# Performance work log

Measured on AMD Instinct MI355X. Metric: run time of the kernel, lower is better.

Reference implementation:

```python
import jax, jax.numpy as jnp
import numpy as np

D = 128
N_DRUG = 200000
N_PROT = 100000
E = 800000


def setup_inputs() -> dict:
    key = jax.random.key(0)
    ks = iter(jax.random.split(key, 64))
    inp = {}
    # initial node embeddings (nn.Embedding init: normal std=0.01)
    inp["x_drug"] = jax.random.normal(next(ks), (N_DRUG, D), jnp.float32) * 0.01
    inp["x_prot"] = jax.random.normal(next(ks), (N_PROT, D), jnp.float32) * 0.01
    # SAGEConv params per (layer, relation): lin_l (weight+bias), lin_r (weight, no bias)
    scale = 1.0 / np.sqrt(D)
    for l in (0, 1):
        for r in ("dp", "pd", "dd"):
            inp[f"Wl_{l}_{r}"] = jax.random.normal(next(ks), (D, D), jnp.float32) * scale
            inp[f"b_{l}_{r}"] = jnp.zeros((D,), jnp.float32)
            inp[f"Wr_{l}_{r}"] = jax.random.normal(next(ks), (D, D), jnp.float32) * scale
    # edge lists: (drug->protein), (protein->drug), (drug->drug)
    inp["e_dp_src"] = jax.random.randint(next(ks), (E,), 0, N_DRUG, dtype=jnp.int32)
    inp["e_dp_dst"] = jax.random.randint(next(ks), (E,), 0, N_PROT, dtype=jnp.int32)
    inp["e_pd_src"] = jax.random.randint(next(ks), (E,), 0, N_PROT, dtype=jnp.int32)
    inp["e_pd_dst"] = jax.random.randint(next(ks), (E,), 0, N_DRUG, dtype=jnp.int32)
    inp["e_dd_src"] = jax.random.randint(next(ks), (E,), 0, N_DRUG, dtype=jnp.int32)
    inp["e_dd_dst"] = jax.random.randint(next(ks), (E,), 0, N_DRUG, dtype=jnp.int32)
    return inp


def _sage(x_src, x_dst, src, dst, Wl, b, Wr):
    """PyG SAGEConv(aggr='mean'): lin_l(mean_neighbors) + lin_r(x_dst)."""
    n_dst = x_dst.shape[0]
    agg = jax.ops.segment_sum(x_src[src], dst, num_segments=n_dst)          # [n_dst, D]
    cnt = jax.ops.segment_sum(jnp.ones(src.shape, x_src.dtype), dst, num_segments=n_dst)
    mean = agg / jnp.maximum(cnt, 1.0)[:, None]  # isolated nodes -> 0
    return mean @ Wl.T + b + x_dst @ Wr.T


def _forward(xd, xp, params, edges):
    e_dp_s, e_dp_d, e_pd_s, e_pd_d, e_dd_s, e_dd_d = edges
    for l in (0, 1):
        p = params[l]
        # HeteroConv(aggr='sum'): sum SAGEConv outputs per destination node type
        new_p = _sage(xd, xp, e_dp_s, e_dp_d, *p["dp"])
        new_d = _sage(xp, xd, e_pd_s, e_pd_d, *p["pd"]) + _sage(xd, xd, e_dd_s, e_dd_d, *p["dd"])
        xd, xp = new_d, new_p
        if l == 0:  # relu (+ dropout as identity in eval) between layers only
            xd, xp = jax.nn.relu(xd), jax.nn.relu(xp)
    return jnp.concatenate([xd, xp], axis=0)  # [N_DRUG + N_PROT, D]


def reference(x_drug, x_prot,
              Wl_0_dp, b_0_dp, Wr_0_dp, Wl_0_pd, b_0_pd, Wr_0_pd, Wl_0_dd, b_0_dd, Wr_0_dd,
              Wl_1_dp, b_1_dp, Wr_1_dp, Wl_1_pd, b_1_pd, Wr_1_pd, Wl_1_dd, b_1_dd, Wr_1_dd,
              e_dp_src, e_dp_dst, e_pd_src, e_pd_dst, e_dd_src, e_dd_dst):
    params = [
        {"dp": (Wl_0_dp, b_0_dp, Wr_0_dp), "pd": (Wl_0_pd, b_0_pd, Wr_0_pd), "dd": (Wl_0_dd, b_0_dd, Wr_0_dd)},
        {"dp": (Wl_1_dp, b_1_dp, Wr_1_dp), "pd": (Wl_1_pd, b_1_pd, Wr_1_pd), "dd": (Wl_1_dd, b_1_dd, Wr_1_dd)},
    ]
    edges = (e_dp_src, e_dp_dst, e_pd_src, e_pd_dst, e_dd_src, e_dd_dst)
    return _forward(x_drug, x_prot, params, edges)
```

## Files before the change

kernel.cpp:

```cpp
#include <hip/hip_runtime.h>

#define D 128

using short8 = __attribute__((ext_vector_type(8))) short;
using f32x4 = __attribute__((ext_vector_type(4))) float;

__device__ inline unsigned short f2bf(float f) {
  unsigned u = __float_as_uint(f);
  u += 0x7fffu + ((u >> 16) & 1u);
  return (unsigned short)(u >> 16);
}

__device__ inline int swz(int r, int kbyte) {
  return ((r << 8) + kbyte) ^ ((r & 7) << 4);
}

__device__ inline unsigned relu_pk(unsigned w) {
  if (w & 0x8000u) w &= 0xffff0000u;
  if (w & 0x80000000u) w &= 0x0000ffffu;
  return w;
}


__global__ __launch_bounds__(256) void count_int_kernel(const int* __restrict__ dst,
                                                        int* __restrict__ cnt, int n) {
  int i = blockIdx.x * 256 + threadIdx.x;
  if (i < n) atomicAdd(&cnt[dst[i]], 1);
}

__global__ __launch_bounds__(256) void blocksum_kernel(const int* __restrict__ cnt,
                                                       int* __restrict__ bsums, int n) {
  __shared__ int sh[256];
  int i = blockIdx.x * 256 + threadIdx.x;
  sh[threadIdx.x] = (i < n) ? cnt[i] : 0;
  __syncthreads();
#pragma unroll
  for (int off = 128; off > 0; off >>= 1) {
    if (threadIdx.x < off) sh[threadIdx.x] += sh[threadIdx.x + off];
    __syncthreads();
  }
  if (threadIdx.x == 0) bsums[blockIdx.x] = sh[0];
}

__global__ __launch_bounds__(256) void scan_bsums_kernel(int* __restrict__ bsums, int nb) {
  __shared__ int sh[256];
  __shared__ int carry;
  if (threadIdx.x == 0) carry = 0;
  __syncthreads();
  for (int base = 0; base < nb; base += 256) {
    int i = base + threadIdx.x;
    int v = (i < nb) ? bsums[i] : 0;
    sh[threadIdx.x] = v;
    __syncthreads();
#pragma unroll
    for (int off = 1; off < 256; off <<= 1) {
      int t = (threadIdx.x >= off) ? sh[threadIdx.x - off] : 0;
      __syncthreads();
      sh[threadIdx.x] += t;
      __syncthreads();
    }
    int incl = sh[threadIdx.x];
    if (i < nb) bsums[i] = carry + incl - v;
    __syncthreads();
    if (threadIdx.x == 0) carry += sh[255];
    __syncthreads();
  }
}

__global__ __launch_bounds__(256) void scan_finalize_kernel(const int* __restrict__ cnt,
                                                            const int* __restrict__ bsums,
                                                            int* __restrict__ rowptr,
                                                            int n, int total) {
  __shared__ int sh[256];
  int i = blockIdx.x * 256 + threadIdx.x;
  int v = (i < n) ? cnt[i] : 0;
  sh[threadIdx.x] = v;
  __syncthreads();
#pragma unroll
  for (int off = 1; off < 256; off <<= 1) {
    int t = (threadIdx.x >= off) ? sh[threadIdx.x - off] : 0;
    __syncthreads();
    sh[threadIdx.x] += t;
    __syncthreads();
  }
  if (i < n) {
    rowptr[i] = bsums[blockIdx.x] + sh[threadIdx.x] - v;
    if (i == n - 1) rowptr[n] = total;
  }
}

__global__ __launch_bounds__(256) void fill_kernel(const int* __restrict__ src,
                                                   const int* __restrict__ dst,
                                                   int* __restrict__ cursor,
                                                   int* __restrict__ slots, int n) {
  int i = blockIdx.x * 256 + threadIdx.x;
  if (i < n) {
    int pos = atomicAdd(&cursor[dst[i]], 1);
    slots[pos] = src[i];
  }
}


template<bool PERM>
__global__ __launch_bounds__(256) void prep_weights_kernel(
    const float* __restrict__ Wrpd, const float* __restrict__ Wrdd,
    const float* __restrict__ Wldd, const float* __restrict__ Wldp,
    const float* __restrict__ Wrdp, const float* __restrict__ Wlpd,
    const float* __restrict__ bpd, const float* __restrict__ bdd,
    unsigned short* __restrict__ Wb, float* __restrict__ bsum) {
  int g = blockIdx.x * 256 + threadIdx.x;
  if (g < 5 * 4096) {
    int mat = g >> 12, idx = g & 4095;
    int c = idx >> 5, k4 = (idx & 31) * 4;
    const float* src0;
    const float* src1 = nullptr;
    switch (mat) {
      case 0: src0 = Wrpd; src1 = Wrdd; break;
      case 1: src0 = Wldd; break;
      case 2: src0 = Wldp; break;
      case 3: src0 = Wrdp; break;
      default: src0 = Wlpd; break;
    }
    unsigned short v[4];
#pragma unroll
    for (int j = 0; j < 4; ++j) {
      int kp = k4 + j;
      int kc = PERM ? ((kp & 7) * 16 + (kp >> 3)) : kp;
      float f = src0[c * D + kc];
      if (src1) f += src1[c * D + kc];
      v[j] = f2bf(f);
    }
    *reinterpret_cast<ushort4*>((char*)(Wb + mat * D * D) + swz(c, k4 * 2)) =
        make_ushort4(v[0], v[1], v[2], v[3]);
  }
  if (g < D) bsum[g] = bpd[g] + bdd[g];
}


template<typename XT, bool RELU>
__device__ inline short8 ld_frag(const XT* __restrict__ p, bool valid) {
  if constexpr (sizeof(XT) == 4) {
    float4 v0 = make_float4(0.f, 0.f, 0.f, 0.f), v1 = v0;
    if (valid) {
      v0 = *reinterpret_cast<const float4*>(p);
      v1 = *reinterpret_cast<const float4*>(p + 4);
    }
    if (RELU) {
      v0.x = fmaxf(v0.x, 0.f); v0.y = fmaxf(v0.y, 0.f);
      v0.z = fmaxf(v0.z, 0.f); v0.w = fmaxf(v0.w, 0.f);
      v1.x = fmaxf(v1.x, 0.f); v1.y = fmaxf(v1.y, 0.f);
      v1.z = fmaxf(v1.z, 0.f); v1.w = fmaxf(v1.w, 0.f);
    }
    short8 s;
    s[0] = (short)f2bf(v0.x); s[1] = (short)f2bf(v0.y);
    s[2] = (short)f2bf(v0.z); s[3] = (short)f2bf(v0.w);
    s[4] = (short)f2bf(v1.x); s[5] = (short)f2bf(v1.y);
    s[6] = (short)f2bf(v1.z); s[7] = (short)f2bf(v1.w);
    return s;
  } else {
    uint4 u = make_uint4(0, 0, 0, 0);
    if (valid) u = *reinterpret_cast<const uint4*>(p);
    if (RELU) { u.x = relu_pk(u.x); u.y = relu_pk(u.y); u.z = relu_pk(u.z); u.w = relu_pk(u.w); }
    union { uint4 u; short8 s; } cv; cv.u = u;
    return cv.s;
  }
}


template<typename XT, bool RELU, int NH, bool OUT0_F32>
__global__ __launch_bounds__(256, 1) void fused_gemm_kernel(
    const XT* __restrict__ X, const unsigned short* __restrict__ Wb,
    const float* __restrict__ bias0, void* __restrict__ out0,
    unsigned short* __restrict__ out1,
    int nrows, int ntiles) {
  __shared__ short Wsh[NH * D * D];
  const int tid = threadIdx.x;

  for (int i = tid; i < NH * 2048; i += 256)
    reinterpret_cast<uint4*>(Wsh)[i] = reinterpret_cast<const uint4*>(Wb)[i];
  __syncthreads();

  const int wv = tid >> 6, lane = tid & 63;
  const int l15 = lane & 15, lg = lane >> 4;
  const int rbase = wv * 32;

  float bias_c[8];
#pragma unroll
  for (int n = 0; n < 8; ++n) bias_c[n] = bias0 ? bias0[n * 16 + l15] : 0.f;

  auto loadA = [&](short8 (&a)[2][4], int tile) {
    size_t row0 = (size_t)tile * 128;
    long rem = (long)nrows - (long)row0;
    int limit = (int)(rem < 128 ? rem : 128);
    bool v0 = (rbase + l15) < limit, v1 = (rbase + l15 + 16) < limit;
    const XT* b0 = X + (row0 + rbase + l15) * D;
    const XT* b1 = X + (row0 + rbase + l15 + 16) * D;
#pragma unroll
    for (int t = 0; t < 4; ++t) {
      int k0 = t * 32 + lg * 8;
      a[0][t] = ld_frag<XT, RELU>(b0 + k0, v0);
      a[1][t] = ld_frag<XT, RELU>(b1 + k0, v1);
    }
  };

  auto store_bf16 = [&](f32x4 (&acc)[2][8], unsigned short* out, size_t row0,
                        int limit, bool addb) {
#pragma unroll
    for (int m = 0; m < 2; ++m)
#pragma unroll
      for (int r = 0; r < 4; ++r) {
        int lrow = rbase + m * 16 + lg * 4 + r;
        if (lrow < limit) {
          float f[8];
#pragma unroll
          for (int n = 0; n < 8; ++n) f[n] = acc[m][n][r] + (addb ? bias_c[n] : 0.f);
          uint4 u;
          u.x = (unsigned)f2bf(f[0]) | ((unsigned)f2bf(f[1]) << 16);
          u.y = (unsigned)f2bf(f[2]) | ((unsigned)f2bf(f[3]) << 16);
          u.z = (unsigned)f2bf(f[4]) | ((unsigned)f2bf(f[5]) << 16);
          u.w = (unsigned)f2bf(f[6]) | ((unsigned)f2bf(f[7]) << 16);
          *reinterpret_cast<uint4*>(out + (row0 + lrow) * D + l15 * 8) = u;
        }
      }
  };

  auto store_f32 = [&](f32x4 (&acc)[2][8], float* out, size_t row0, int limit) {
#pragma unroll
    for (int m = 0; m < 2; ++m)
#pragma unroll
      for (int n = 0; n < 8; ++n) {
        const int col = n * 16 + l15;
#pragma unroll
        for (int r = 0; r < 4; ++r) {
          int lrow = rbase + m * 16 + lg * 4 + r;
          if (lrow < limit) out[(row0 + lrow) * D + col] = acc[m][n][r] + bias_c[n];
        }
      }
  };

  auto do_tile = [&](short8 (&acur)[2][4], short8 (&anext)[2][4], int tile) {
    int ntile = tile + (int)gridDim.x;
    if (ntile < ntiles) loadA(anext, ntile);

    size_t row0 = (size_t)tile * 128;
    long rem = (long)nrows - (long)row0;
    int limit = (int)(rem < 128 ? rem : 128);

#pragma unroll
    for (int h = 0; h < NH; ++h) {
      f32x4 acc[2][8] = {};
#pragma unroll
      for (int t = 0; t < 4; ++t) {
        const int kb = t * 64 + lg * 16;
        const char* base = (const char*)(Wsh + h * D * D);
#pragma unroll
        for (int n = 0; n < 8; ++n) {
          short8 b = *reinterpret_cast<const short8*>(base + swz(n * 16 + l15, kb));
          acc[0][n] = __builtin_amdgcn_mfma_f32_16x16x32_bf16(acur[0][t], b, acc[0][n], 0, 0, 0);
          acc[1][n] = __builtin_amdgcn_mfma_f32_16x16x32_bf16(acur[1][t], b, acc[1][n], 0, 0, 0);
        }
      }
      if (h == 0) {
        if (OUT0_F32) store_f32(acc, (float*)out0, row0, limit);
        else          store_bf16(acc, (unsigned short*)out0, row0, limit, true);
      } else {
        store_bf16(acc, out1, row0, limit, false);
      }
    }
  };

  short8 aA[2][4], aB[2][4];
  int tile = blockIdx.x;
  if (tile >= ntiles) return;
  loadA(aA, tile);
  while (true) {
    do_tile(aA, aB, tile);
    tile += gridDim.x;
    if (tile >= ntiles) break;
    do_tile(aB, aA, tile);
    tile += gridDim.x;
    if (tile >= ntiles) break;
  }
}


__device__ inline void addbf8(float* sum, uint4 v) {
  sum[0] += __uint_as_float(v.x << 16);
  sum[1] += __uint_as_float(v.x & 0xffff0000u);
  sum[2] += __uint_as_float(v.y << 16);
  sum[3] += __uint_as_float(v.y & 0xffff0000u);
  sum[4] += __uint_as_float(v.z << 16);
  sum[5] += __uint_as_float(v.z & 0xffff0000u);
  sum[6] += __uint_as_float(v.w << 16);
  sum[7] += __uint_as_float(v.w & 0xffff0000u);
}

__device__ inline float gather_one(const uint4* __restrict__ Y4,
                                   const int* __restrict__ rowptr,
                                   const int* __restrict__ slots,
                                   int node, int lane, float* sum) {
  int s0 = rowptr[node], s1 = rowptr[node + 1];
  for (int chunk = s0; chunk < s1; chunk += 16) {
    int idx = chunk + lane;
    int pre = (idx < s1) ? slots[idx] : 0;
    int m = s1 - chunk; if (m > 16) m = 16;
    int j = 0;
    for (; j + 4 <= m; j += 4) {
      int sA = __shfl(pre, j, 16);
      int sB = __shfl(pre, j + 1, 16);
      int sC = __shfl(pre, j + 2, 16);
      int sD = __shfl(pre, j + 3, 16);
      uint4 vA = Y4[(size_t)sA * 16 + lane];
      uint4 vB = Y4[(size_t)sB * 16 + lane];
      uint4 vC = Y4[(size_t)sC * 16 + lane];
      uint4 vD = Y4[(size_t)sD * 16 + lane];
      addbf8(sum, vA); addbf8(sum, vB); addbf8(sum, vC); addbf8(sum, vD);
    }
    for (; j < m; ++j) {
      int s = __shfl(pre, j, 16);
      addbf8(sum, Y4[(size_t)s * 16 + lane]);
    }
  }
  return 1.0f / fmaxf((float)(s1 - s0), 1.0f);
}

template<int NREL, int MODE>
__global__ __launch_bounds__(256) void gatherN_kernel(
    const unsigned short* __restrict__ Y0, const int* __restrict__ rp0, const int* __restrict__ sl0,
    const unsigned short* __restrict__ Y1, const int* __restrict__ rp1, const int* __restrict__ sl1,
    void* __restrict__ acc, int nnodes) {
  long g = (long)blockIdx.x * 256 + threadIdx.x;
  int node = (int)(g >> 4);
  if (node >= nnodes) return;
  int lane = (int)(g & 15);

  float t0[8] = {}, t1[8] = {};
  float inv0 = gather_one(reinterpret_cast<const uint4*>(Y0), rp0, sl0, node, lane, t0);
  float inv1 = 0.f;
  if (NREL == 2)
    inv1 = gather_one(reinterpret_cast<const uint4*>(Y1), rp1, sl1, node, lane, t1);

  if (MODE == 1) {
    unsigned short* ap = (unsigned short*)acc + (size_t)node * D + lane * 8;
    uint4 u = *reinterpret_cast<uint4*>(ap);
    float a[8];
    a[0] = __uint_as_float(u.x << 16); a[1] = __uint_as_float(u.x & 0xffff0000u);
    a[2] = __uint_as_float(u.y << 16); a[3] = __uint_as_float(u.y & 0xffff0000u);
    a[4] = __uint_as_float(u.z << 16); a[5] = __uint_as_float(u.z & 0xffff0000u);
    a[6] = __uint_as_float(u.w << 16); a[7] = __uint_as_float(u.w & 0xffff0000u);
#pragma unroll
    for (int i = 0; i < 8; ++i) {
      a[i] += t0[i] * inv0;
      if (NREL == 2) a[i] += t1[i] * inv1;
    }
    uint4 o;
    o.x = (unsigned)f2bf(a[0]) | ((unsigned)f2bf(a[1]) << 16);
    o.y = (unsigned)f2bf(a[2]) | ((unsigned)f2bf(a[3]) << 16);
    o.z = (unsigned)f2bf(a[4]) | ((unsigned)f2bf(a[5]) << 16);
    o.w = (unsigned)f2bf(a[6]) | ((unsigned)f2bf(a[7]) << 16);
    *reinterpret_cast<uint4*>(ap) = o;
  } else {
    float* ap = (float*)acc + (size_t)node * D + lane;
#pragma unroll
    for (int i = 0; i < 8; ++i) {
      float a = ap[i * 16];
      a += t0[i] * inv0;
      if (NREL == 2) a += t1[i] * inv1;
      ap[i * 16] = a;
    }
  }
}


extern "C" void kernel_launch(void* const* d_in, const int* in_sizes, int n_in,
                              void* d_out, int out_size, void* d_ws, size_t ws_size,
                              hipStream_t stream) {
  const float* x_drug = (const float*)d_in[0];
  const float* x_prot = (const float*)d_in[1];
  const float* Wl0dp = (const float*)d_in[2];  const float* b0dp = (const float*)d_in[3];  const float* Wr0dp = (const float*)d_in[4];
  const float* Wl0pd = (const float*)d_in[5];  const float* b0pd = (const float*)d_in[6];  const float* Wr0pd = (const float*)d_in[7];
  const float* Wl0dd = (const float*)d_in[8];  const float* b0dd = (const float*)d_in[9];  const float* Wr0dd = (const float*)d_in[10];
  const float* Wl1dp = (const float*)d_in[11]; const float* b1dp = (const float*)d_in[12]; const float* Wr1dp = (const float*)d_in[13];
  const float* Wl1pd = (const float*)d_in[14]; const float* b1pd = (const float*)d_in[15]; const float* Wr1pd = (const float*)d_in[16];
  const float* Wl1dd = (const float*)d_in[17]; const float* b1dd = (const float*)d_in[18]; const float* Wr1dd = (const float*)d_in[19];
  const int* e_dp_s = (const int*)d_in[20]; const int* e_dp_d = (const int*)d_in[21];
  const int* e_pd_s = (const int*)d_in[22]; const int* e_pd_d = (const int*)d_in[23];
  const int* e_dd_s = (const int*)d_in[24]; const int* e_dd_d = (const int*)d_in[25];

  const int ND = in_sizes[0] / D;
  const int NP = in_sizes[1] / D;
  const int E_dp = in_sizes[20], E_pd = in_sizes[22], E_dd = in_sizes[24];

  unsigned short* accD  = (unsigned short*)d_ws;
  unsigned short* accP  = accD + (size_t)ND * D;
  unsigned short* bufdd = accP + (size_t)NP * D;
  unsigned short* bufdp = bufdd + (size_t)ND * D;
  unsigned short* bufpd = bufdp + (size_t)ND * D;
  unsigned short* Wb    = bufpd + (size_t)NP * D;
  float* bsum  = (float*)(Wb + 5 * D * D);
  int* rp_dp  = (int*)(bsum + D);
  int* rp_pd  = rp_dp + (NP + 2);
  int* rp_dd  = rp_pd + (ND + 2);
  int* sl_dp  = rp_dd + (ND + 2);
  int* sl_pd  = sl_dp + E_dp;
  int* sl_dd  = sl_pd + E_pd;
  int* cnt    = sl_dd + E_dd;
  int* bsums  = cnt + ND;

  auto cdiv = [](long a, long b) { return (int)((a + b - 1) / b); };

  auto build_csr = [&](const int* esrc, const int* edst, int ne, int ndst,
                       int* rowptr, int* slots) {
    int nb = cdiv(ndst, 256);
    hipMemsetAsync(cnt, 0, (size_t)ndst * sizeof(int), stream);
    count_int_kernel<<<cdiv(ne, 256), 256, 0, stream>>>(edst, cnt, ne);
    blocksum_kernel<<<nb, 256, 0, stream>>>(cnt, bsums, ndst);
    scan_bsums_kernel<<<1, 256, 0, stream>>>(bsums, nb);
    scan_finalize_kernel<<<nb, 256, 0, stream>>>(cnt, bsums, rowptr, ndst, ne);
    hipMemcpyAsync(cnt, rowptr, (size_t)ndst * sizeof(int), hipMemcpyDeviceToDevice, stream);
    fill_kernel<<<cdiv(ne, 256), 256, 0, stream>>>(esrc, edst, cnt, slots, ne);
  };

  build_csr(e_dp_s, e_dp_d, E_dp, NP, rp_dp, sl_dp);
  build_csr(e_pd_s, e_pd_d, E_pd, ND, rp_pd, sl_pd);
  build_csr(e_dd_s, e_dd_d, E_dd, ND, rp_dd, sl_dd);

  const int tilesD = cdiv(ND, 128), tilesP = cdiv(NP, 128);

  prep_weights_kernel<false><<<80, 256, 0, stream>>>(
      Wr0pd, Wr0dd, Wl0dd, Wl0dp, Wr0dp, Wl0pd, b0pd, b0dd, Wb, bsum);
  fused_gemm_kernel<float, false, 2, false><<<512, 256, 0, stream>>>(
      x_drug, Wb, bsum, accD, bufdd, ND, tilesD);
  fused_gemm_kernel<float, false, 1, false><<<512, 256, 0, stream>>>(
      x_drug, Wb + 2 * D * D, nullptr, bufdp, nullptr, ND, tilesD);
  fused_gemm_kernel<float, false, 2, false><<<512, 256, 0, stream>>>(
      x_prot, Wb + 3 * D * D, b0dp, accP, bufpd, NP, tilesP);
  gatherN_kernel<2, 1><<<cdiv((long)ND * 16, 256), 256, 0, stream>>>(
      bufpd, rp_pd, sl_pd, bufdd, rp_dd, sl_dd, accD, ND);
  gatherN_kernel<1, 1><<<cdiv((long)NP * 16, 256), 256, 0, stream>>>(
      bufdp, rp_dp, sl_dp, nullptr, nullptr, nullptr, accP, NP);

  float* outD1 = (float*)d_out;
  float* outP1 = outD1 + (size_t)ND * D;
  prep_weights_kernel<true><<<80, 256, 0, stream>>>(
      Wr1pd, Wr1dd, Wl1dd, Wl1dp, Wr1dp, Wl1pd, b1pd, b1dd, Wb, bsum);
  fused_gemm_kernel<unsigned short, true, 2, true><<<512, 256, 0, stream>>>(
      accD, Wb, bsum, outD1, bufdd, ND, tilesD);
  fused_gemm_kernel<unsigned short, true, 1, false><<<512, 256, 0, stream>>>(
      accD, Wb + 2 * D * D, nullptr, bufdp, nullptr, ND, tilesD);
  fused_gemm_kernel<unsigned short, true, 2, true><<<512, 256, 0, stream>>>(
      accP, Wb + 3 * D * D, b1dp, outP1, bufpd, NP, tilesP);
  gatherN_kernel<2, 0><<<cdiv((long)ND * 16, 256), 256, 0, stream>>>(
      bufpd, rp_pd, sl_pd, bufdd, rp_dd, sl_dd, outD1, ND);
  gatherN_kernel<1, 0><<<cdiv((long)NP * 16, 256), 256, 0, stream>>>(
      bufdp, rp_dp, sl_dp, nullptr, nullptr, nullptr, outP1, NP);
}
```

Measured before the change: 819.8 us.

## Aggregate neighbor means before the linear transform and fuse the three GEMM heads

Reorders each SAGE layer so that neighbor means are gathered first, from the raw or ReLU'd node features. The linear weights are then applied in a single sum_gemm kernel that accumulates the self, pd and dd terms in one accumulator and writes the output once. This removes the intermediate transformed buffers and the read-modify-write of the accumulator (fp32 in the final layer) that the gather used to perform. In exchange, the layer-0 gather now reads fp32 rows, twice the bytes of the old bf16 transformed rows. The fused GEMM also loads three activation inputs and keeps 96KB of weights in LDS on only 256 blocks.

```diff
diff --git a/kernel.cpp b/kernel.cpp
--- a/kernel.cpp
+++ b/kernel.cpp
@@ -104,8 +104,8 @@
 template<bool PERM>
 __global__ __launch_bounds__(256) void prep_weights_kernel(
     const float* __restrict__ Wrpd, const float* __restrict__ Wrdd,
-    const float* __restrict__ Wldd, const float* __restrict__ Wldp,
-    const float* __restrict__ Wrdp, const float* __restrict__ Wlpd,
+    const float* __restrict__ Wlpd, const float* __restrict__ Wldd,
+    const float* __restrict__ Wrdp, const float* __restrict__ Wldp,
     const float* __restrict__ bpd, const float* __restrict__ bdd,
     unsigned short* __restrict__ Wb, float* __restrict__ bsum) {
   int g = blockIdx.x * 256 + threadIdx.x;
@@ -116,10 +116,10 @@
     const float* src1 = nullptr;
     switch (mat) {
       case 0: src0 = Wrpd; src1 = Wrdd; break;
-      case 1: src0 = Wldd; break;
-      case 2: src0 = Wldp; break;
+      case 1: src0 = Wlpd; break;
+      case 2: src0 = Wldd; break;
       case 3: src0 = Wrdp; break;
-      default: src0 = Wlpd; break;
+      default: src0 = Wldp; break;
     }
     unsigned short v[4];
 #pragma unroll
@@ -167,12 +167,12 @@
 }
 
 
-template<typename XT, bool RELU, int NH, bool OUT0_F32>
-__global__ __launch_bounds__(256, 1) void fused_gemm_kernel(
-    const XT* __restrict__ X, const unsigned short* __restrict__ Wb,
-    const float* __restrict__ bias0, void* __restrict__ out0,
-    unsigned short* __restrict__ out1,
-    int nrows, int ntiles) {
+template<typename XT0, bool RELU0, int NH, bool OUT_F32>
+__global__ __launch_bounds__(256, 1) void sum_gemm_kernel(
+    const XT0* __restrict__ X0, const unsigned short* __restrict__ X1,
+    const unsigned short* __restrict__ X2,
+    const unsigned short* __restrict__ Wb, const float* __restrict__ bias0,
+    void* __restrict__ out, int nrows, int ntiles) {
   __shared__ short Wsh[NH * D * D];
   const int tid = threadIdx.x;
 
@@ -186,100 +186,110 @@
 
   float bias_c[8];
 #pragma unroll
-  for (int n = 0; n < 8; ++n) bias_c[n] = bias0 ? bias0[n * 16 + l15] : 0.f;
-
-  auto loadA = [&](short8 (&a)[2][4], int tile) {
+  for (int n = 0; n < 8; ++n) bias_c[n] = bias0[n * 16 + l15];
+
+  auto load0 = [&](short8 (&a)[2][4], int tile) {
     size_t row0 = (size_t)tile * 128;
     long rem = (long)nrows - (long)row0;
     int limit = (int)(rem < 128 ? rem : 128);
     bool v0 = (rbase + l15) < limit, v1 = (rbase + l15 + 16) < limit;
-    const XT* b0 = X + (row0 + rbase + l15) * D;
-    const XT* b1 = X + (row0 + rbase + l15 + 16) * D;
+    const XT0* b0 = X0 + (row0 + rbase + l15) * D;
+    const XT0* b1 = X0 + (row0 + rbase + l15 + 16) * D;
 #pragma unroll
     for (int t = 0; t < 4; ++t) {
       int k0 = t * 32 + lg * 8;
-      a[0][t] = ld_frag<XT, RELU>(b0 + k0, v0);
-      a[1][t] = ld_frag<XT, RELU>(b1 + k0, v1);
+      a[0][t] = ld_frag<XT0, RELU0>(b0 + k0, v0);
+      a[1][t] = ld_frag<XT0, RELU0>(b1 + k0, v1);
     }
   };
-
-  auto store_bf16 = [&](f32x4 (&acc)[2][8], unsigned short* out, size_t row0,
-                        int limit, bool addb) {
-#pragma unroll
-    for (int m = 0; m < 2; ++m)
-#pragma unroll
-      for (int r = 0; r < 4; ++r) {
-        int lrow = rbase + m * 16 + lg * 4 + r;
-        if (lrow < limit) {
-          float f[8];
-#pragma unroll
-          for (int n = 0; n < 8; ++n) f[n] = acc[m][n][r] + (addb ? bias_c[n] : 0.f);
-          uint4 u;
-          u.x = (unsigned)f2bf(f[0]) | ((unsigned)f2bf(f[1]) << 16);
-          u.y = (unsigned)f2bf(f[2]) | ((unsigned)f2bf(f[3]) << 16);
-          u.z = (unsigned)f2bf(f[4]) | ((unsigned)f2bf(f[5]) << 16);
-          u.w = (unsigned)f2bf(f[6]) | ((unsigned)f2bf(f[7]) << 16);
-          *reinterpret_cast<uint4*>(out + (row0 + lrow) * D + l15 * 8) = u;
-        }
-      }
-  };
-
-  auto store_f32 = [&](f32x4 (&acc)[2][8], float* out, size_t row0, int limit) {
-#pragma unroll
-    for (int m = 0; m < 2; ++m)
-#pragma unroll
-      for (int n = 0; n < 8; ++n) {
-        const int col = n * 16 + l15;
-#pragma unroll
-        for (int r = 0; r < 4; ++r) {
-          int lrow = rbase + m * 16 + lg * 4 + r;
-          if (lrow < limit) out[(row0 + lrow) * D + col] = acc[m][n][r] + bias_c[n];
-        }
-      }
-  };
-
-  auto do_tile = [&](short8 (&acur)[2][4], short8 (&anext)[2][4], int tile) {
-    int ntile = tile + (int)gridDim.x;
-    if (ntile < ntiles) loadA(anext, ntile);
-
+  auto loadM = [&](short8 (&a)[2][4], const unsigned short* Xm, int tile) {
     size_t row0 = (size_t)tile * 128;
     long rem = (long)nrows - (long)row0;
     int limit = (int)(rem < 128 ? rem : 128);
-
-#pragma unroll
-    for (int h = 0; h < NH; ++h) {
-      f32x4 acc[2][8] = {};
-#pragma unroll
-      for (int t = 0; t < 4; ++t) {
-        const int kb = t * 64 + lg * 16;
-        const char* base = (const char*)(Wsh + h * D * D);
-#pragma unroll
-        for (int n = 0; n < 8; ++n) {
-          short8 b = *reinterpret_cast<const short8*>(base + swz(n * 16 + l15, kb));
-          acc[0][n] = __builtin_amdgcn_mfma_f32_16x16x32_bf16(acur[0][t], b, acc[0][n], 0, 0, 0);
-          acc[1][n] = __builtin_amdgcn_mfma_f32_16x16x32_bf16(acur[1][t], b, acc[1][n], 0, 0, 0);
-        }
+    bool v0 = (rbase + l15) < limit, v1 = (rbase + l15 + 16) < limit;
+    const unsigned short* b0 = Xm + (row0 + rbase + l15) * D;
+    const unsigned short* b1 = Xm + (row0 + rbase + l15 + 16) * D;
+#pragma unroll
+    for (int t = 0; t < 4; ++t) {
+      int k0 = t * 32 + lg * 8;
+      a[0][t] = ld_frag<unsigned short, false>(b0 + k0, v0);
+      a[1][t] = ld_frag<unsigned short, false>(b1 + k0, v1);
+    }
+  };
+
+  auto mfma_head = [&](short8 (&B)[2][4], const short* wbase, f32x4 (&acc)[2][8]) {
+#pragma unroll
+    for (int t = 0; t < 4; ++t) {
+      const int kb = t * 64 + lg * 16;
+#pragma unroll
+      for (int n = 0; n < 8; ++n) {
+        short8 b = *reinterpret_cast<const short8*>((const char*)wbase + swz(n * 16 + l15, kb));
+        acc[0][n] = __builtin_amdgcn_mfma_f32_16x16x32_bf16(B[0][t], b, acc[0][n], 0, 0, 0);
+        acc[1][n] = __builtin_amdgcn_mfma_f32_16x16x32_bf16(B[1][t], b, acc[1][n], 0, 0, 0);
       }
-      if (h == 0) {
-        if (OUT0_F32) store_f32(acc, (float*)out0, row0, limit);
-        else          store_bf16(acc, (unsigned short*)out0, row0, limit, true);
-      } else {
-        store_bf16(acc, out1, row0, limit, false);
-      }
     }
   };
 
-  short8 aA[2][4], aB[2][4];
+  short8 B0[2][4], B1[2][4], B2[2][4];
   int tile = blockIdx.x;
   if (tile >= ntiles) return;
-  loadA(aA, tile);
+  load0(B0, tile);
+  loadM(B1, X1, tile);
+  if constexpr (NH == 3) loadM(B2, X2, tile);
+
   while (true) {
-    do_tile(aA, aB, tile);
-    tile += gridDim.x;
-    if (tile >= ntiles) break;
-    do_tile(aB, aA, tile);
-    tile += gridDim.x;
-    if (tile >= ntiles) break;
+    size_t row0 = (size_t)tile * 128;
+    long rem = (long)nrows - (long)row0;
+    int limit = (int)(rem < 128 ? rem : 128);
+    int nt = tile + (int)gridDim.x;
+    bool hn = nt < ntiles;
+
+    f32x4 acc[2][8] = {};
+    mfma_head(B0, Wsh, acc);
+    if (hn) load0(B0, nt);
+    mfma_head(B1, Wsh + D * D, acc);
+    if (hn) loadM(B1, X1, nt);
+    if constexpr (NH == 3) {
+      mfma_head(B2, Wsh + 2 * D * D, acc);
+      if (hn) loadM(B2, X2, nt);
+    }
+
+    if (OUT_F32) {
+      float* o = (float*)out;
+#pragma unroll
+      for (int m = 0; m < 2; ++m)
+#pragma unroll
+        for (int n = 0; n < 8; ++n) {
+          const int col = n * 16 + l15;
+#pragma unroll
+          for (int r = 0; r < 4; ++r) {
+            int lrow = rbase + m * 16 + lg * 4 + r;
+            if (lrow < limit) o[(row0 + lrow) * D + col] = acc[m][n][r] + bias_c[n];
+          }
+        }
+    } else {
+      unsigned short* o = (unsigned short*)out;
+#pragma unroll
+      for (int m = 0; m < 2; ++m)
+#pragma unroll
+        for (int r = 0; r < 4; ++r) {
+          int lrow = rbase + m * 16 + lg * 4 + r;
+          if (lrow < limit) {
+            float f[8];
+#pragma unroll
+            for (int n = 0; n < 8; ++n) f[n] = acc[m][n][r] + bias_c[n];
+            uint4 u;
+            u.x = (unsigned)f2bf(f[0]) | ((unsigned)f2bf(f[1]) << 16);
+            u.y = (unsigned)f2bf(f[2]) | ((unsigned)f2bf(f[3]) << 16);
+            u.z = (unsigned)f2bf(f[4]) | ((unsigned)f2bf(f[5]) << 16);
+            u.w = (unsigned)f2bf(f[6]) | ((unsigned)f2bf(f[7]) << 16);
+            *reinterpret_cast<uint4*>(o + (row0 + lrow) * D + l15 * 8) = u;
+          }
+        }
+    }
+
+    if (!hn) break;
+    tile = nt;
   }
 }
 
@@ -295,7 +305,27 @@
   sum[7] += __uint_as_float(v.w & 0xffff0000u);
 }
 
-__device__ inline float gather_one(const uint4* __restrict__ Y4,
+template<typename ST, bool RELU>
+__device__ inline void add_row(const ST* __restrict__ Y, int s, int lane, float* sum) {
+  if constexpr (sizeof(ST) == 4) {
+    const float4* F = reinterpret_cast<const float4*>(Y);
+    float4 p = F[(size_t)s * 32 + lane * 2];
+    float4 q = F[(size_t)s * 32 + lane * 2 + 1];
+    if (RELU) {
+      p.x = fmaxf(p.x, 0.f); p.y = fmaxf(p.y, 0.f); p.z = fmaxf(p.z, 0.f); p.w = fmaxf(p.w, 0.f);
+      q.x = fmaxf(q.x, 0.f); q.y = fmaxf(q.y, 0.f); q.z = fmaxf(q.z, 0.f); q.w = fmaxf(q.w, 0.f);
+    }
+    sum[0] += p.x; sum[1] += p.y; sum[2] += p.z; sum[3] += p.w;
+    sum[4] += q.x; sum[5] += q.y; sum[6] += q.z; sum[7] += q.w;
+  } else {
+    uint4 v = reinterpret_cast<const uint4*>(Y)[(size_t)s * 16 + lane];
+    if (RELU) { v.x = relu_pk(v.x); v.y = relu_pk(v.y); v.z = relu_pk(v.z); v.w = relu_pk(v.w); }
+    addbf8(sum, v);
+  }
+}
+
+template<typename ST, bool RELU>
+__device__ inline float gather_one(const ST* __restrict__ Y,
                                    const int* __restrict__ rowptr,
                                    const int* __restrict__ slots,
                                    int node, int lane, float* sum) {
@@ -310,64 +340,47 @@
       int sB = __shfl(pre, j + 1, 16);
       int sC = __shfl(pre, j + 2, 16);
       int sD = __shfl(pre, j + 3, 16);
-      uint4 vA = Y4[(size_t)sA * 16 + lane];
-      uint4 vB = Y4[(size_t)sB * 16 + lane];
-      uint4 vC = Y4[(size_t)sC * 16 + lane];
-      uint4 vD = Y4[(size_t)sD * 16 + lane];
-      addbf8(sum, vA); addbf8(sum, vB); addbf8(sum, vC); addbf8(sum, vD);
+      add_row<ST, RELU>(Y, sA, lane, sum);
+      add_row<ST, RELU>(Y, sB, lane, sum);
+      add_row<ST, RELU>(Y, sC, lane, sum);
+      add_row<ST, RELU>(Y, sD, lane, sum);
     }
     for (; j < m; ++j) {
       int s = __shfl(pre, j, 16);
-      addbf8(sum, Y4[(size_t)s * 16 + lane]);
+      add_row<ST, RELU>(Y, s, lane, sum);
     }
   }
   return 1.0f / fmaxf((float)(s1 - s0), 1.0f);
 }
 
-template<int NREL, int MODE>
-__global__ __launch_bounds__(256) void gatherN_kernel(
-    const unsigned short* __restrict__ Y0, const int* __restrict__ rp0, const int* __restrict__ sl0,
-    const unsigned short* __restrict__ Y1, const int* __restrict__ rp1, const int* __restrict__ sl1,
-    void* __restrict__ acc, int nnodes) {
+__device__ inline uint4 pack8(const float* t, float inv) {
+  uint4 o;
+  o.x = (unsigned)f2bf(t[0] * inv) | ((unsigned)f2bf(t[1] * inv) << 16);
+  o.y = (unsigned)f2bf(t[2] * inv) | ((unsigned)f2bf(t[3] * inv) << 16);
+  o.z = (unsigned)f2bf(t[4] * inv) | ((unsigned)f2bf(t[5] * inv) << 16);
+  o.w = (unsigned)f2bf(t[6] * inv) | ((unsigned)f2bf(t[7] * inv) << 16);
+  return o;
+}
+
+template<int NREL, typename ST, bool RELU>
+__global__ __launch_bounds__(256) void gather_mean_kernel(
+    const ST* __restrict__ Y0, const int* __restrict__ rp0, const int* __restrict__ sl0,
+    unsigned short* __restrict__ out0,
+    const ST* __restrict__ Y1, const int* __restrict__ rp1, const int* __restrict__ sl1,
+    unsigned short* __restrict__ out1, int nnodes) {
   long g = (long)blockIdx.x * 256 + threadIdx.x;
   int node = (int)(g >> 4);
   if (node >= nnodes) return;
   int lane = (int)(g & 15);
 
-  float t0[8] = {}, t1[8] = {};
-  float inv0 = gather_one(reinterpret_cast<const uint4*>(Y0), rp0, sl0, node, lane, t0);
-  float inv1 = 0.f;
-  if (NREL == 2)
-    inv1 = gather_one(reinterpret_cast<const uint4*>(Y1), rp1, sl1, node, lane, t1);
-
-  if (MODE == 1) {
-    unsigned short* ap = (unsigned short*)acc + (size_t)node * D + lane * 8;
-    uint4 u = *reinterpret_cast<uint4*>(ap);
-    float a[8];
-    a[0] = __uint_as_float(u.x << 16); a[1] = __uint_as_float(u.x & 0xffff0000u);
-    a[2] = __uint_as_float(u.y << 16); a[3] = __uint_as_float(u.y & 0xffff0000u);
-    a[4] = __uint_as_float(u.z << 16); a[5] = __uint_as_float(u.z & 0xffff0000u);
-    a[6] = __uint_as_float(u.w << 16); a[7] = __uint_as_float(u.w & 0xffff0000u);
-#pragma unroll
-    for (int i = 0; i < 8; ++i) {
-      a[i] += t0[i] * inv0;
-      if (NREL == 2) a[i] += t1[i] * inv1;
-    }
-    uint4 o;
-    o.x = (unsigned)f2bf(a[0]) | ((unsigned)f2bf(a[1]) << 16);
-    o.y = (unsigned)f2bf(a[2]) | ((unsigned)f2bf(a[3]) << 16);
-    o.z = (unsigned)f2bf(a[4]) | ((unsigned)f2bf(a[5]) << 16);
-    o.w = (unsigned)f2bf(a[6]) | ((unsigned)f2bf(a[7]) << 16);
-    *reinterpret_cast<uint4*>(ap) = o;
-  } else {
-    float* ap = (float*)acc + (size_t)node * D + lane;
-#pragma unroll
-    for (int i = 0; i < 8; ++i) {
-      float a = ap[i * 16];
-      a += t0[i] * inv0;
-      if (NREL == 2) a += t1[i] * inv1;
-      ap[i * 16] = a;
-    }
+  float t0[8] = {};
+  float inv0 = gather_one<ST, RELU>(Y0, rp0, sl0, node, lane, t0);
+  *reinterpret_cast<uint4*>(out0 + (size_t)node * D + lane * 8) = pack8(t0, inv0);
+
+  if (NREL == 2) {
+    float t1[8] = {};
+    float inv1 = gather_one<ST, RELU>(Y1, rp1, sl1, node, lane, t1);
+    *reinterpret_cast<uint4*>(out1 + (size_t)node * D + lane * 8) = pack8(t1, inv1);
   }
 }
 
@@ -391,13 +404,13 @@
   const int NP = in_sizes[1] / D;
   const int E_dp = in_sizes[20], E_pd = in_sizes[22], E_dd = in_sizes[24];
 
-  unsigned short* accD  = (unsigned short*)d_ws;
-  unsigned short* accP  = accD + (size_t)ND * D;
-  unsigned short* bufdd = accP + (size_t)NP * D;
-  unsigned short* bufdp = bufdd + (size_t)ND * D;
-  unsigned short* bufpd = bufdp + (size_t)ND * D;
-  unsigned short* Wb    = bufpd + (size_t)NP * D;
-  float* bsum  = (float*)(Wb + 5 * D * D);
+  unsigned short* accD = (unsigned short*)d_ws;
+  unsigned short* accP = accD + (size_t)ND * D;
+  unsigned short* m_pd = accP + (size_t)NP * D;
+  unsigned short* m_dd = m_pd + (size_t)ND * D;
+  unsigned short* m_dp = m_dd + (size_t)ND * D;
+  unsigned short* Wb   = m_dp + (size_t)NP * D;
+  float* bsum = (float*)(Wb + 5 * D * D);
   int* rp_dp  = (int*)(bsum + D);
   int* rp_pd  = rp_dp + (NP + 2);
   int* rp_dd  = rp_pd + (ND + 2);
@@ -426,32 +439,29 @@
   build_csr(e_dd_s, e_dd_d, E_dd, ND, rp_dd, sl_dd);
 
   const int tilesD = cdiv(ND, 128), tilesP = cdiv(NP, 128);
+  const int gD = cdiv((long)ND * 16, 256), gP = cdiv((long)NP * 16, 256);
 
   prep_weights_kernel<false><<<80, 256, 0, stream>>>(
-      Wr0pd, Wr0dd, Wl0dd, Wl0dp, Wr0dp, Wl0pd, b0pd, b0dd, Wb, bsum);
-  fused_gemm_kernel<float, false, 2, false><<<512, 256, 0, stream>>>(
-      x_drug, Wb, bsum, accD, bufdd, ND, tilesD);
-  fused_gemm_kernel<float, false, 1, false><<<512, 256, 0, stream>>>(
-      x_drug, Wb + 2 * D * D, nullptr, bufdp, nullptr, ND, tilesD);
-  fused_gemm_kernel<float, false, 2, false><<<512, 256, 0, stream>>>(
-      x_prot, Wb + 3 * D * D, b0dp, accP, bufpd, NP, tilesP);
-  gatherN_kernel<2, 1><<<cdiv((long)ND * 16, 256), 256, 0, stream>>>(
-      bufpd, rp_pd, sl_pd, bufdd, rp_dd, sl_dd, accD, ND);
-  gatherN_kernel<1, 1><<<cdiv((long)NP * 16, 256), 256, 0, stream>>>(
-      bufdp, rp_dp, sl_dp, nullptr, nullptr, nullptr, accP, NP);
+      Wr0pd, Wr0dd, Wl0pd, Wl0dd, Wr0dp, Wl0dp, b0pd, b0dd, Wb, bsum);
+  gather_mean_kernel<2, float, false><<<gD, 256, 0, stream>>>(
+      x_prot, rp_pd, sl_pd, m_pd, x_drug, rp_dd, sl_dd, m_dd, ND);
+  gather_mean_kernel<1, float, false><<<gP, 256, 0, stream>>>(
+      x_drug, rp_dp, sl_dp, m_dp, nullptr, nullptr, nullptr, nullptr, NP);
+  sum_gemm_kernel<float, false, 3, false><<<256, 256, 0, stream>>>(
+      x_drug, m_pd, m_dd, Wb, bsum, accD, ND, tilesD);
+  sum_gemm_kernel<float, false, 2, false><<<512, 256, 0, stream>>>(
+      x_prot, m_dp, nullptr, Wb + 3 * D * D, b0dp, accP, NP, tilesP);
 
   float* outD1 = (float*)d_out;
   float* outP1 = outD1 + (size_t)ND * D;
   prep_weights_kernel<true><<<80, 256, 0, stream>>>(
-      Wr1pd, Wr1dd, Wl1dd, Wl1dp, Wr1dp, Wl1pd, b1pd, b1dd, Wb, bsum);
-  fused_gemm_kernel<unsigned short, true, 2, true><<<512, 256, 0, stream>>>(
-      accD, Wb, bsum, outD1, bufdd, ND, tilesD);
-  fused_gemm_kernel<unsigned short, true, 1, false><<<512, 256, 0, stream>>>(
-      accD, Wb + 2 * D * D, nullptr, bufdp, nullptr, ND, tilesD);
-  fused_gemm_kernel<unsigned short, true, 2, true><<<512, 256, 0, stream>>>(
-      accP, Wb + 3 * D * D, b1dp, outP1, bufpd, NP, tilesP);
-  gatherN_kernel<2, 0><<<cdiv((long)ND * 16, 256), 256, 0, stream>>>(
-      bufpd, rp_pd, sl_pd, bufdd, rp_dd, sl_dd, outD1, ND);
-  gatherN_kernel<1, 0><<<cdiv((long)NP * 16, 256), 256, 0, stream>>>(
-      bufdp, rp_dp, sl_dp, nullptr, nullptr, nullptr, outP1, NP);
-}
+      Wr1pd, Wr1dd, Wl1pd, Wl1dd, Wr1dp, Wl1dp, b1pd, b1dd, Wb, bsum);
+  gather_mean_kernel<2, unsigned short, true><<<gD, 256, 0, stream>>>(
+      accP, rp_pd, sl_pd, m_pd, accD, rp_dd, sl_dd, m_dd, ND);
+  gather_mean_kernel<1, unsigned short, true><<<gP, 256, 0, stream>>>(
+      accD, rp_dp, sl_dp, m_dp, nullptr, nullptr, nullptr, nullptr, NP);
+  sum_gemm_kernel<unsigned short, true, 3, true><<<256, 256, 0, stream>>>(
+      accD, m_pd, m_dd, Wb, bsum, outD1, ND, tilesD);
+  sum_gemm_kernel<unsigned short, true, 2, true><<<512, 256, 0, stream>>>(
+      accP, m_dp, nullptr, Wb + 3 * D * D, b1dp, outP1, NP, tilesP);
+}
```

New measurement: 945.8 us. 1.15x slower.

## Aggregate-then-transform in layer two and fuse heads into summed GEMM

Applied to the files above, without the earlier changes.

Layer two now gathers neighbour means of the raw (ReLU'd) layer-one features first, then runs a single GEMM kernel per node type that multiplies self, mean-pd and mean-dd inputs by their weights and accumulates them, writing the fp32 output once. This replaces the transform-then-gather scheme that wrote transformed bf16 buffers and did read-modify-write on the fp32 output in the gather. It removes intermediate GEMM outputs and the separate fp32 accumulate pass, at the cost of a 3-head GEMM that needs 96KB of LDS for weights and uses only 256 blocks.

```diff
diff --git a/kernel.cpp b/kernel.cpp
--- a/kernel.cpp
+++ b/kernel.cpp
@@ -103,9 +103,9 @@
 
 template<bool PERM>
 __global__ __launch_bounds__(256) void prep_weights_kernel(
-    const float* __restrict__ Wrpd, const float* __restrict__ Wrdd,
-    const float* __restrict__ Wldd, const float* __restrict__ Wldp,
-    const float* __restrict__ Wrdp, const float* __restrict__ Wlpd,
+    const float* __restrict__ W0a, const float* __restrict__ W0b,
+    const float* __restrict__ W1, const float* __restrict__ W2,
+    const float* __restrict__ W3, const float* __restrict__ W4,
     const float* __restrict__ bpd, const float* __restrict__ bdd,
     unsigned short* __restrict__ Wb, float* __restrict__ bsum) {
   int g = blockIdx.x * 256 + threadIdx.x;
@@ -115,11 +115,11 @@
     const float* src0;
     const float* src1 = nullptr;
     switch (mat) {
-      case 0: src0 = Wrpd; src1 = Wrdd; break;
-      case 1: src0 = Wldd; break;
-      case 2: src0 = Wldp; break;
-      case 3: src0 = Wrdp; break;
-      default: src0 = Wlpd; break;
+      case 0: src0 = W0a; src1 = W0b; break;
+      case 1: src0 = W1; break;
+      case 2: src0 = W2; break;
+      case 3: src0 = W3; break;
+      default: src0 = W4; break;
     }
     unsigned short v[4];
 #pragma unroll
@@ -167,10 +167,10 @@
 }
 
 
-template<typename XT, bool RELU, int NH, bool OUT0_F32>
+template<typename XT, bool RELU, int NH>
 __global__ __launch_bounds__(256, 1) void fused_gemm_kernel(
     const XT* __restrict__ X, const unsigned short* __restrict__ Wb,
-    const float* __restrict__ bias0, void* __restrict__ out0,
+    const float* __restrict__ bias0, unsigned short* __restrict__ out0,
     unsigned short* __restrict__ out1,
     int nrows, int ntiles) {
   __shared__ short Wsh[NH * D * D];
@@ -224,20 +224,6 @@
       }
   };
 
-  auto store_f32 = [&](f32x4 (&acc)[2][8], float* out, size_t row0, int limit) {
-#pragma unroll
-    for (int m = 0; m < 2; ++m)
-#pragma unroll
-      for (int n = 0; n < 8; ++n) {
-        const int col = n * 16 + l15;
-#pragma unroll
-        for (int r = 0; r < 4; ++r) {
-          int lrow = rbase + m * 16 + lg * 4 + r;
-          if (lrow < limit) out[(row0 + lrow) * D + col] = acc[m][n][r] + bias_c[n];
-        }
-      }
-  };
-
   auto do_tile = [&](short8 (&acur)[2][4], short8 (&anext)[2][4], int tile) {
     int ntile = tile + (int)gridDim.x;
     if (ntile < ntiles) loadA(anext, ntile);
@@ -260,12 +246,8 @@
           acc[1][n] = __builtin_amdgcn_mfma_f32_16x16x32_bf16(acur[1][t], b, acc[1][n], 0, 0, 0);
         }
       }
-      if (h == 0) {
-        if (OUT0_F32) store_f32(acc, (float*)out0, row0, limit);
-        else          store_bf16(acc, (unsigned short*)out0, row0, limit, true);
-      } else {
-        store_bf16(acc, out1, row0, limit, false);
-      }
+      if (h == 0) store_bf16(acc, out0, row0, limit, true);
+      else        store_bf16(acc, out1, row0, limit, false);
     }
   };
 
@@ -284,6 +266,102 @@
 }
 
 
+template<int NH>
+__global__ __launch_bounds__(256, 1) void sum_gemm_kernel(
+    const unsigned short* __restrict__ X0, const unsigned short* __restrict__ X1,
+    const unsigned short* __restrict__ X2,
+    const unsigned short* __restrict__ Wb, const float* __restrict__ bias0,
+    float* __restrict__ out, int nrows, int ntiles) {
+  __shared__ short Wsh[NH * D * D];
+  const int tid = threadIdx.x;
+
+  for (int i = tid; i < NH * 2048; i += 256)
+    reinterpret_cast<uint4*>(Wsh)[i] = reinterpret_cast<const uint4*>(Wb)[i];
+  __syncthreads();
+
+  const int wv = tid >> 6, lane = tid & 63;
+  const int l15 = lane & 15, lg = lane >> 4;
+  const int rbase = wv * 32;
+
+  float bias_c[8];
+#pragma unroll
+  for (int n = 0; n < 8; ++n) bias_c[n] = bias0[n * 16 + l15];
+
+  auto loadX = [&](short8 (&a)[2][4], const unsigned short* Xm, int tile, bool relu) {
+    size_t row0 = (size_t)tile * 128;
+    long rem = (long)nrows - (long)row0;
+    int limit = (int)(rem < 128 ? rem : 128);
+    bool v0 = (rbase + l15) < limit, v1 = (rbase + l15 + 16) < limit;
+    const unsigned short* b0 = Xm + (row0 + rbase + l15) * D;
+    const unsigned short* b1 = Xm + (row0 + rbase + l15 + 16) * D;
+#pragma unroll
+    for (int t = 0; t < 4; ++t) {
+      int k0 = t * 32 + lg * 8;
+      if (relu) {
+        a[0][t] = ld_frag<unsigned short, true>(b0 + k0, v0);
+        a[1][t] = ld_frag<unsigned short, true>(b1 + k0, v1);
+      } else {
+        a[0][t] = ld_frag<unsigned short, false>(b0 + k0, v0);
+        a[1][t] = ld_frag<unsigned short, false>(b1 + k0, v1);
+      }
+    }
+  };
+
+  auto mfma_head = [&](short8 (&B)[2][4], const short* wbase, f32x4 (&acc)[2][8]) {
+#pragma unroll
+    for (int t = 0; t < 4; ++t) {
+      const int kb = t * 64 + lg * 16;
+#pragma unroll
+      for (int n = 0; n < 8; ++n) {
+        short8 b = *reinterpret_cast<const short8*>((const char*)wbase + swz(n * 16 + l15, kb));
+        acc[0][n] = __builtin_amdgcn_mfma_f32_16x16x32_bf16(B[0][t], b, acc[0][n], 0, 0, 0);
+        acc[1][n] = __builtin_amdgcn_mfma_f32_16x16x32_bf16(B[1][t], b, acc[1][n], 0, 0, 0);
+      }
+    }
+  };
+
+  short8 B0[2][4], B1[2][4], B2[2][4];
+  int tile = blockIdx.x;
+  if (tile >= ntiles) return;
+  loadX(B0, X0, tile, true);
+  loadX(B1, X1, tile, false);
+  if constexpr (NH == 3) loadX(B2, X2, tile, false);
+
+  while (true) {
+    size_t row0 = (size_t)tile * 128;
+    long rem = (long)nrows - (long)row0;
+    int limit = (int)(rem < 128 ? rem : 128);
+    int nt = tile + (int)gridDim.x;
+    bool hn = nt < ntiles;
+
+    f32x4 acc[2][8] = {};
+    mfma_head(B0, Wsh, acc);
+    if (hn) loadX(B0, X0, nt, true);
+    mfma_head(B1, Wsh + D * D, acc);
+    if (hn) loadX(B1, X1, nt, false);
+    if constexpr (NH == 3) {
+      mfma_head(B2, Wsh + 2 * D * D, acc);
+      if (hn) loadX(B2, X2, nt, false);
+    }
+
+#pragma unroll
+    for (int m = 0; m < 2; ++m)
+#pragma unroll
+      for (int n = 0; n < 8; ++n) {
+        const int col = n * 16 + l15;
+#pragma unroll
+        for (int r = 0; r < 4; ++r) {
+          int lrow = rbase + m * 16 + lg * 4 + r;
+          if (lrow < limit) out[(row0 + lrow) * D + col] = acc[m][n][r] + bias_c[n];
+        }
+      }
+
+    if (!hn) break;
+    tile = nt;
+  }
+}
+
+
 __device__ inline void addbf8(float* sum, uint4 v) {
   sum[0] += __uint_as_float(v.x << 16);
   sum[1] += __uint_as_float(v.x & 0xffff0000u);
@@ -295,7 +373,16 @@
   sum[7] += __uint_as_float(v.w & 0xffff0000u);
 }
 
-__device__ inline float gather_one(const uint4* __restrict__ Y4,
+template<bool RELU>
+__device__ inline void add_row(const unsigned short* __restrict__ Y, int s, int lane,
+                               float* sum) {
+  uint4 v = reinterpret_cast<const uint4*>(Y)[(size_t)s * 16 + lane];
+  if (RELU) { v.x = relu_pk(v.x); v.y = relu_pk(v.y); v.z = relu_pk(v.z); v.w = relu_pk(v.w); }
+  addbf8(sum, v);
+}
+
+template<bool RELU>
+__device__ inline float gather_one(const unsigned short* __restrict__ Y,
                                    const int* __restrict__ rowptr,
                                    const int* __restrict__ slots,
                                    int node, int lane, float* sum) {
@@ -310,64 +397,82 @@
       int sB = __shfl(pre, j + 1, 16);
       int sC = __shfl(pre, j + 2, 16);
       int sD = __shfl(pre, j + 3, 16);
-      uint4 vA = Y4[(size_t)sA * 16 + lane];
-      uint4 vB = Y4[(size_t)sB * 16 + lane];
-      uint4 vC = Y4[(size_t)sC * 16 + lane];
-      uint4 vD = Y4[(size_t)sD * 16 + lane];
-      addbf8(sum, vA); addbf8(sum, vB); addbf8(sum, vC); addbf8(sum, vD);
+      add_row<RELU>(Y, sA, lane, sum);
+      add_row<RELU>(Y, sB, lane, sum);
+      add_row<RELU>(Y, sC, lane, sum);
+      add_row<RELU>(Y, sD, lane, sum);
     }
     for (; j < m; ++j) {
       int s = __shfl(pre, j, 16);
-      addbf8(sum, Y4[(size_t)s * 16 + lane]);
+      add_row<RELU>(Y, s, lane, sum);
     }
   }
   return 1.0f / fmaxf((float)(s1 - s0), 1.0f);
 }
 
-template<int NREL, int MODE>
+__device__ inline uint4 pack8(const float* t, float inv) {
+  uint4 o;
+  o.x = (unsigned)f2bf(t[0] * inv) | ((unsigned)f2bf(t[1] * inv) << 16);
+  o.y = (unsigned)f2bf(t[2] * inv) | ((unsigned)f2bf(t[3] * inv) << 16);
+  o.z = (unsigned)f2bf(t[4] * inv) | ((unsigned)f2bf(t[5] * inv) << 16);
+  o.w = (unsigned)f2bf(t[6] * inv) | ((unsigned)f2bf(t[7] * inv) << 16);
+  return o;
+}
+
+template<int NREL>
 __global__ __launch_bounds__(256) void gatherN_kernel(
     const unsigned short* __restrict__ Y0, const int* __restrict__ rp0, const int* __restrict__ sl0,
     const unsigned short* __restrict__ Y1, const int* __restrict__ rp1, const int* __restrict__ sl1,
-    void* __restrict__ acc, int nnodes) {
+    unsigned short* __restrict__ acc, int nnodes) {
   long g = (long)blockIdx.x * 256 + threadIdx.x;
   int node = (int)(g >> 4);
   if (node >= nnodes) return;
   int lane = (int)(g & 15);
 
   float t0[8] = {}, t1[8] = {};
-  float inv0 = gather_one(reinterpret_cast<const uint4*>(Y0), rp0, sl0, node, lane, t0);
+  float inv0 = gather_one<false>(Y0, rp0, sl0, node, lane, t0);
   float inv1 = 0.f;
-  if (NREL == 2)
-    inv1 = gather_one(reinterpret_cast<const uint4*>(Y1), rp1, sl1, node, lane, t1);
-
-  if (MODE == 1) {
-    unsigned short* ap = (unsigned short*)acc + (size_t)node * D + lane * 8;
-    uint4 u = *reinterpret_cast<uint4*>(ap);
-    float a[8];
-    a[0] = __uint_as_float(u.x << 16); a[1] = __uint_as_float(u.x & 0xffff0000u);
-    a[2] = __uint_as_float(u.y << 16); a[3] = __uint_as_float(u.y & 0xffff0000u);
-    a[4] = __uint_as_float(u.z << 16); a[5] = __uint_as_float(u.z & 0xffff0000u);
-    a[6] = __uint_as_float(u.w << 16); a[7] = __uint_as_float(u.w & 0xffff0000u);
-#pragma unroll
-    for (int i = 0; i < 8; ++i) {
-      a[i] += t0[i] * inv0;
-      if (NREL == 2) a[i] += t1[i] * inv1;
-    }
-    uint4 o;
-    o.x = (unsigned)f2bf(a[0]) | ((unsigned)f2bf(a[1]) << 16);
-    o.y = (unsigned)f2bf(a[2]) | ((unsigned)f2bf(a[3]) << 16);
-    o.z = (unsigned)f2bf(a[4]) | ((unsigned)f2bf(a[5]) << 16);
-    o.w = (unsigned)f2bf(a[6]) | ((unsigned)f2bf(a[7]) << 16);
-    *reinterpret_cast<uint4*>(ap) = o;
-  } else {
-    float* ap = (float*)acc + (size_t)node * D + lane;
-#pragma unroll
-    for (int i = 0; i < 8; ++i) {
-      float a = ap[i * 16];
-      a += t0[i] * inv0;
-      if (NREL == 2) a += t1[i] * inv1;
-      ap[i * 16] = a;
-    }
+  if (NREL == 2) inv1 = gather_one<false>(Y1, rp1, sl1, node, lane, t1);
+
+  unsigned short* ap = acc + (size_t)node * D + lane * 8;
+  uint4 u = *reinterpret_cast<uint4*>(ap);
+  float a[8];
+  a[0] = __uint_as_float(u.x << 16); a[1] = __uint_as_float(u.x & 0xffff0000u);
+  a[2] = __uint_as_float(u.y << 16); a[3] = __uint_as_float(u.y & 0xffff0000u);
+  a[4] = __uint_as_float(u.z << 16); a[5] = __uint_as_float(u.z & 0xffff0000u);
+  a[6] = __uint_as_float(u.w << 16); a[7] = __uint_as_float(u.w & 0xffff0000u);
+#pragma unroll
+  for (int i = 0; i < 8; ++i) {
+    a[i] += t0[i] * inv0;
+    if (NREL == 2) a[i] += t1[i] * inv1;
+  }
+  uint4 o;
+  o.x = (unsigned)f2bf(a[0]) | ((unsigned)f2bf(a[1]) << 16);
+  o.y = (unsigned)f2bf(a[2]) | ((unsigned)f2bf(a[3]) << 16);
+  o.z = (unsigned)f2bf(a[4]) | ((unsigned)f2bf(a[5]) << 16);
+  o.w = (unsigned)f2bf(a[6]) | ((unsigned)f2bf(a[7]) << 16);
+  *reinterpret_cast<uint4*>(ap) = o;
+}
+
+template<int NREL>
+__global__ __launch_bounds__(256) void gather_mean_kernel(
+    const unsigned short* __restrict__ Y0, const int* __restrict__ rp0, const int* __restrict__ sl0,
+    unsigned short* __restrict__ out0,
+    const unsigned short* __restrict__ Y1, const int* __restrict__ rp1, const int* __restrict__ sl1,
+    unsigned short* __restrict__ out1, int nnodes) {
+  long g = (long)blockIdx.x * 256 + threadIdx.x;
+  int node = (int)(g >> 4);
+  if (node >= nnodes) return;
+  int lane = (int)(g & 15);
+
+  float t0[8] = {};
+  float inv0 = gather_one<true>(Y0, rp0, sl0, node, lane, t0);
+  *reinterpret_cast<uint4*>(out0 + (size_t)node * D + lane * 8) = pack8(t0, inv0);
+
+  if (NREL == 2) {
+    float t1[8] = {};
+    float inv1 = gather_one<true>(Y1, rp1, sl1, node, lane, t1);
+    *reinterpret_cast<uint4*>(out1 + (size_t)node * D + lane * 8) = pack8(t1, inv1);
   }
 }
 
@@ -397,7 +502,7 @@
   unsigned short* bufdp = bufdd + (size_t)ND * D;
   unsigned short* bufpd = bufdp + (size_t)ND * D;
   unsigned short* Wb    = bufpd + (size_t)NP * D;
-  float* bsum  = (float*)(Wb + 5 * D * D);
+  float* bsum = (float*)(Wb + 5 * D * D);
   int* rp_dp  = (int*)(bsum + D);
   int* rp_pd  = rp_dp + (NP + 2);
   int* rp_dd  = rp_pd + (ND + 2);
@@ -406,6 +511,10 @@
   int* sl_dd  = sl_pd + E_pd;
   int* cnt    = sl_dd + E_dd;
   int* bsums  = cnt + ND;
+
+  unsigned short* m_pd = bufdd;
+  unsigned short* m_dd = bufdp;
+  unsigned short* m_dp = bufpd;
 
   auto cdiv = [](long a, long b) { return (int)((a + b - 1) / b); };
 
@@ -426,32 +535,31 @@
   build_csr(e_dd_s, e_dd_d, E_dd, ND, rp_dd, sl_dd);
 
   const int tilesD = cdiv(ND, 128), tilesP = cdiv(NP, 128);
+  const int gD = cdiv((long)ND * 16, 256), gP = cdiv((long)NP * 16, 256);
 
   prep_weights_kernel<false><<<80, 256, 0, stream>>>(
       Wr0pd, Wr0dd, Wl0dd, Wl0dp, Wr0dp, Wl0pd, b0pd, b0dd, Wb, bsum);
-  fused_gemm_kernel<float, false, 2, false><<<512, 256, 0, stream>>>(
+  fused_gemm_kernel<float, false, 2><<<512, 256, 0, stream>>>(
       x_drug, Wb, bsum, accD, bufdd, ND, tilesD);
-  fused_gemm_kernel<float, false, 1, false><<<512, 256, 0, stream>>>(
+  fused_gemm_kernel<float, false, 1><<<512, 256, 0, stream>>>(
       x_drug, Wb + 2 * D * D, nullptr, bufdp, nullptr, ND, tilesD);
-  fused_gemm_kernel<float, false, 2, false><<<512, 256, 0, stream>>>(
+  fused_gemm_kernel<float, false, 2><<<512, 256, 0, stream>>>(
       x_prot, Wb + 3 * D * D, b0dp, accP, bufpd, NP, tilesP);
-  gatherN_kernel<2, 1><<<cdiv((long)ND * 16, 256), 256, 0, stream>>>(
+  gatherN_kernel<2><<<gD, 256, 0, stream>>>(
       bufpd, rp_pd, sl_pd, bufdd, rp_dd, sl_dd, accD, ND);
-  gatherN_kernel<1, 1><<<cdiv((long)NP * 16, 256), 256, 0, stream>>>(
+  gatherN_kernel<1><<<gP, 256, 0, stream>>>(
       bufdp, rp_dp, sl_dp, nullptr, nullptr, nullptr, accP, NP);
 
   float* outD1 = (float*)d_out;
   float* outP1 = outD1 + (size_t)ND * D;
   prep_weights_kernel<true><<<80, 256, 0, stream>>>(
-      Wr1pd, Wr1dd, Wl1dd, Wl1dp, Wr1dp, Wl1pd, b1pd, b1dd, Wb, bsum);
-  fused_gemm_kernel<unsigned short, true, 2, true><<<512, 256, 0, stream>>>(
-      accD, Wb, bsum, outD1, bufdd, ND, tilesD);
-  fused_gemm_kernel<unsigned short, true, 1, false><<<512, 256, 0, stream>>>(
-      accD, Wb + 2 * D * D, nullptr, bufdp, nullptr, ND, tilesD);
-  fused_gemm_kernel<unsigned short, true, 2, true><<<512, 256, 0, stream>>>(
-      accP, Wb + 3 * D * D, b1dp, outP1, bufpd, NP, tilesP);
-  gatherN_kernel<2, 0><<<cdiv((long)ND * 16, 256), 256, 0, stream>>>(
-      bufpd, rp_pd, sl_pd, bufdd, rp_dd, sl_dd, outD1, ND);
-  gatherN_kernel<1, 0><<<cdiv((long)NP * 16, 256), 256, 0, stream>>>(
-      bufdp, rp_dp, sl_dp, nullptr, nullptr, nullptr, outP1, NP);
-}
+      Wr1pd, Wr1dd, Wl1pd, Wl1dd, Wr1dp, Wl1dp, b1pd, b1dd, Wb, bsum);
+  gather_mean_kernel<2><<<gD, 256, 0, stream>>>(
+      accP, rp_pd, sl_pd, m_pd, accD, rp_dd, sl_dd, m_dd, ND);
+  gather_mean_kernel<1><<<gP, 256, 0, stream>>>(
+      accD, rp_dp, sl_dp, m_dp, nullptr, nullptr, nullptr, nullptr, NP);
+  sum_gemm_kernel<3><<<256, 256, 0, stream>>>(
+      accD, m_pd, m_dd, Wb, bsum, outD1, ND, tilesD);
+  sum_gemm_kernel<2><<<512, 256, 0, stream>>>(
+      accP, m_dp, nullptr, Wb + 3 * D * D, b1dp, outP1, NP, tilesP);
+}
```

Result: slower. 847.4 us (+3.4%).
